# Performance work log

Measured on AMD Instinct MI355X. Metric: run time of the kernel, lower is better.

## Reference

```python
import jax, jax.numpy as jnp
import numpy as np

N = 50000           # num_nodes
E = 400000          # num directed input edges
CON_DIM = 128
STRUC_DIM = 64
HIDDEN = 128
NUM_NODE_UPDATES = 5
MAX_GROUP_ITERS = 100


def setup_inputs() -> dict:
    key = jax.random.key(0)
    k = jax.random.split(key, 5)
    return {
        "con_feats": jax.random.normal(k[0], (N, CON_DIM), jnp.float32),
        "struc_feats": jax.random.normal(k[1], (N, STRUC_DIM), jnp.float32),
        "W1": jax.random.normal(k[2], (2 * CON_DIM, HIDDEN), jnp.float32) * 0.05,
        "b1": jnp.zeros((HIDDEN,), jnp.float32),
        "W2": jax.random.normal(k[3], (HIDDEN, 1), jnp.float32) * 0.05,
        "b2": jnp.zeros((1,), jnp.float32),
        "edge_ids": jax.random.randint(k[4], (2, E), 0, N, jnp.int32),
    }


def _edge_scores(con_feats, W1, b1, W2, b2, src, dst, upper):
    # MLP edge scorer on concatenated endpoint features; relu'd score,
    # zeroed on edges failing the dst > src pruning (equivalent to torch's
    # boolean pruning: score-0 edges contribute nothing downstream).
    x = jnp.concatenate([con_feats[src], con_feats[dst]], axis=1)  # [E, 2*C]
    raw = (jax.nn.relu(x @ W1 + b1) @ W2 + b2)[:, 0]               # [E]
    return jax.nn.relu(raw) * upper


def reference(con_feats, struc_feats, W1, b1, W2, b2, edge_ids):
    num_nodes = con_feats.shape[0]
    src, dst = edge_ids[0], edge_ids[1]
    upper = (dst > src).astype(con_feats.dtype)
    scores = _edge_scores(con_feats, W1, b1, W2, b2, src, dst, upper)
    ar = jnp.arange(num_nodes, dtype=edge_ids.dtype)

    # full edge set: pruned + flipped + self-loops (score-0 edges are no-ops)
    all_src = jnp.concatenate([src, dst, ar])
    all_dst = jnp.concatenate([dst, src, ar])
    all_scores = jnp.concatenate([scores, scores, jnp.ones((num_nodes,), scores.dtype)])

    # row-wise normalization (scatter-sum over source node)
    node_sums = jax.ops.segment_sum(all_scores, all_src, num_segments=num_nodes)
    norm_scores = all_scores / node_sums[all_src]

    def spmm(f):  # sparse [N,N] @ dense [N,d]
        return jax.ops.segment_sum(norm_scores[:, None] * f[all_dst], all_src,
                                   num_segments=num_nodes)

    for _ in range(NUM_NODE_UPDATES):
        con_feats = spmm(con_feats)
        struc_feats = spmm(struc_feats)

    # connected-components label propagation over edges with positive score
    # (edges with score==0 are rewritten as self-edges instead of filtered,
    # which is a no-op for scatter-min; self-loops appended as in torch)
    g_src = jnp.concatenate([jnp.where(scores > 0, src, dst), ar])
    g_dst = jnp.concatenate([dst, ar])

    def cond(state):
        i, _, changed = state
        return (i < MAX_GROUP_ITERS) & changed

    def body(state):
        i, g, _ = state
        new = jax.ops.segment_min(g[g_src], g_dst, num_segments=num_nodes)
        return (i + 1, new, jnp.any(new != g))

    _, group_ids, _ = jax.lax.while_loop(cond, body,
                                         (jnp.int32(0), ar, jnp.bool_(True)))

    # compact labels (torch.unique return_inverse); output padded to N rows
    _, inv = jnp.unique(group_ids, return_inverse=True, size=num_nodes,
                        fill_value=num_nodes - 1)
    inv = inv.reshape(-1)

    counts = jax.ops.segment_sum(jnp.ones((num_nodes,), con_feats.dtype), inv,
                                 num_segments=num_nodes)
    denom = jnp.maximum(counts, 1.0)[:, None]
    con_out = jax.ops.segment_sum(con_feats, inv, num_segments=num_nodes) / denom
    struc_out = jax.ops.segment_sum(struc_feats, inv, num_segments=num_nodes) / denom
    # [N, CON_DIM + STRUC_DIM]; rows >= num_groups are zero padding
    return jnp.concatenate([con_out, struc_out], axis=1)
```

## Files before the change

kernel.cpp:

```cpp
#include <hip/hip_runtime.h>
#include <hip/hip_fp16.h>
#include <cstdint>
#include <cstddef>


__global__ void k_init(const float* __restrict__ con, const float* __restrict__ str,
                       __half* __restrict__ F, float* __restrict__ sums,
                       int* __restrict__ cnt, int* __restrict__ g, int N) {
  int i = blockIdx.x * blockDim.x + threadIdx.x;
  int total = N * 192;
  if (i < total) {
    int n = i / 192, f = i - n * 192;
    float v = (f < 128) ? con[n * 128 + f] : str[n * 64 + (f - 128)];
    F[i] = __float2half_rn(v);
  }
  if (i < N) { sums[i] = 1.0f; cnt[i] = 1; g[i] = i; }
}

__global__ __launch_bounds__(256) void k_proj(const float* __restrict__ con,
                                              const float* __restrict__ W1,
                                              const float* __restrict__ b1,
                                              float* __restrict__ PQf,
                                              __half* __restrict__ PQh, int N) {
  __shared__ float cs[16][128];
  int n0 = blockIdx.x * 16;
  for (int t = threadIdx.x; t < 16 * 128; t += 256) {
    int tn = t >> 7, k = t & 127;
    int node = n0 + tn;
    cs[tn][k] = (node < N) ? con[node * 128 + k] : 0.0f;
  }
  __syncthreads();
  int j = threadIdx.x;
  int base = (j < 128) ? j : (128 * 128 + (j - 128));
  float acc[16];
#pragma unroll
  for (int t = 0; t < 16; ++t) acc[t] = 0.0f;
  float w0 = W1[base + 0 * 128];
  float w1 = W1[base + 1 * 128];
  float w2 = W1[base + 2 * 128];
  float w3 = W1[base + 3 * 128];
  for (int k = 0; k < 128; k += 4) {
    float n0w = 0.f, n1w = 0.f, n2w = 0.f, n3w = 0.f;
    if (k < 124) {
      n0w = W1[base + (k + 4) * 128];
      n1w = W1[base + (k + 5) * 128];
      n2w = W1[base + (k + 6) * 128];
      n3w = W1[base + (k + 7) * 128];
    }
#pragma unroll
    for (int t = 0; t < 16; ++t) {
      const float4 c = *reinterpret_cast<const float4*>(&cs[t][k]);
      acc[t] += c.x * w0 + c.y * w1 + c.z * w2 + c.w * w3;
    }
    w0 = n0w; w1 = n1w; w2 = n2w; w3 = n3w;
  }
  float bj = (j < 128) ? b1[j] : 0.0f;
#pragma unroll
  for (int t = 0; t < 16; ++t) {
    int node = n0 + t;
    if (node < N) {
      float v = acc[t] + bj;
      PQf[(size_t)node * 256 + j] = v;
      PQh[(size_t)node * 256 + j] = __float2half_rn(v);
    }
  }
}

__global__ __launch_bounds__(256) void k_edge(const int* __restrict__ src, const int* __restrict__ dst,
                                              const __half* __restrict__ PQ,
                                              const float* __restrict__ PQf,
                                              const float* __restrict__ W2,
                                              const float* __restrict__ b2,
                                              float* __restrict__ scores,
                                              float* __restrict__ sums, int* __restrict__ cnt,
                                              int* __restrict__ pos_s, int* __restrict__ pos_d,
                                              int* __restrict__ pos_cnt, int E) {
  int e = blockIdx.x * 256 + threadIdx.x;
  bool live = (e < E);
  int s = 0, d = 0;
  if (live) { s = src[e]; d = dst[e]; }
  bool scored = live && (d > s);
  float raw = -1.0f;
  if (scored) {
    const uint4* P = (const uint4*)(PQ + (size_t)s * 256);
    const uint4* Q = (const uint4*)(PQ + (size_t)d * 256 + 128);
    const float4* W = (const float4*)W2;
    float acc = 0.0f;
#pragma unroll 8
    for (int k = 0; k < 16; ++k) {
      uint4 pu = P[k];
      uint4 qu = Q[k];
      float4 wa = W[2 * k], wb = W[2 * k + 1];
      float2 p0 = __half22float2(*(const __half2*)&pu.x);
      float2 p1 = __half22float2(*(const __half2*)&pu.y);
      float2 p2 = __half22float2(*(const __half2*)&pu.z);
      float2 p3 = __half22float2(*(const __half2*)&pu.w);
      float2 q0 = __half22float2(*(const __half2*)&qu.x);
      float2 q1 = __half22float2(*(const __half2*)&qu.y);
      float2 q2 = __half22float2(*(const __half2*)&qu.z);
      float2 q3 = __half22float2(*(const __half2*)&qu.w);
      acc += fmaxf(p0.x + q0.x, 0.f) * wa.x + fmaxf(p0.y + q0.y, 0.f) * wa.y
           + fmaxf(p1.x + q1.x, 0.f) * wa.z + fmaxf(p1.y + q1.y, 0.f) * wa.w
           + fmaxf(p2.x + q2.x, 0.f) * wb.x + fmaxf(p2.y + q2.y, 0.f) * wb.y
           + fmaxf(p3.x + q3.x, 0.f) * wb.z + fmaxf(p3.y + q3.y, 0.f) * wb.w;
    }
    raw = acc + b2[0];
    if (fabsf(raw) < 3e-3f) {
      const float4* Pf = (const float4*)(PQf + (size_t)s * 256);
      const float4* Qf = (const float4*)(PQf + (size_t)d * 256 + 128);
      float acc2 = 0.0f;
      for (int k = 0; k < 32; ++k) {
        float4 p = Pf[k], q = Qf[k], w = W[k];
        acc2 += fmaxf(p.x + q.x, 0.f) * w.x + fmaxf(p.y + q.y, 0.f) * w.y
              + fmaxf(p.z + q.z, 0.f) * w.z + fmaxf(p.w + q.w, 0.f) * w.w;
      }
      raw = acc2 + b2[0];
    }
  }
  float sc = scored ? fmaxf(raw, 0.0f) : 0.0f;
  if (live) scores[e] = sc;
  bool pos = scored && (sc > 0.0f);
  if (pos) {
    atomicAdd(&sums[s], sc);
    atomicAdd(&sums[d], sc);
    atomicAdd(&cnt[s], 1);
    atomicAdd(&cnt[d], 1);
  }
  unsigned long long m = __ballot(pos);
  if (pos) {
    int lane = threadIdx.x & 63;
    int rank = __popcll(m & ((1ULL << lane) - 1));
    int leader = __ffsll((long long)m) - 1;
    int bcast;
    if (lane == leader) bcast = atomicAdd(pos_cnt, __popcll(m));
    bcast = __shfl(bcast, leader, 64);
    pos_s[bcast + rank] = s;
    pos_d[bcast + rank] = d;
  }
}

__device__ __forceinline__ int wave_iscan(int v) {
  int l = threadIdx.x & 63;
#pragma unroll
  for (int o = 1; o < 64; o <<= 1) {
    int t = __shfl_up(v, o, 64);
    if (l >= o) v += t;
  }
  return v;
}

__global__ __launch_bounds__(1024) void k_scan_red(int mode, const int* __restrict__ cnt,
                                                   const int* __restrict__ g,
                                                   int* __restrict__ bsum, int N) {
  __shared__ int wsum[16];
  int i = blockIdx.x * 1024 + threadIdx.x;
  int v = 0;
  if (i < N) v = (mode == 0) ? cnt[i] : ((g[i] == i) ? 1 : 0);
  int incl = wave_iscan(v);
  int wid = threadIdx.x >> 6;
  if ((threadIdx.x & 63) == 63) wsum[wid] = incl;
  __syncthreads();
  if (threadIdx.x == 0) {
    int t = 0;
#pragma unroll
    for (int k = 0; k < 16; ++k) t += wsum[k];
    bsum[blockIdx.x] = t;
  }
}

__global__ __launch_bounds__(64) void k_scan_mid(int mode, const int* __restrict__ bsum,
                                                 int* __restrict__ bexcl, int NB,
                                                 int* __restrict__ rowp, int N) {
  int l = threadIdx.x;
  int v = (l < NB) ? bsum[l] : 0;
  int incl = wave_iscan(v);
  if (l < NB) bexcl[l] = incl - v;
  if (l == 63 && mode == 0) rowp[N] = incl;
}

__global__ __launch_bounds__(1024) void k_scan_out(int mode, const int* __restrict__ cnt,
                                                   const int* __restrict__ g,
                                                   const float* __restrict__ sums,
                                                   const int* __restrict__ bexcl,
                                                   int* __restrict__ rowp, int* __restrict__ fillp,
                                                   int* __restrict__ col, float* __restrict__ wt,
                                                   int* __restrict__ rank, int N) {
  __shared__ int wsum[16];
  int i = blockIdx.x * 1024 + threadIdx.x;
  int v = 0;
  if (i < N) v = (mode == 0) ? cnt[i] : ((g[i] == i) ? 1 : 0);
  int incl = wave_iscan(v);
  int wid = threadIdx.x >> 6;
  if ((threadIdx.x & 63) == 63) wsum[wid] = incl;
  __syncthreads();
  if (threadIdx.x < 64) {
    int l = threadIdx.x;
    int sv = (l < 16) ? wsum[l] : 0;
#pragma unroll
    for (int o = 1; o < 16; o <<= 1) {
      int t = __shfl_up(sv, o, 64);
      if (l >= o) sv += t;
    }
    if (l < 16) wsum[l] = sv;
  }
  __syncthreads();
  int wexcl = (wid == 0) ? 0 : wsum[wid - 1];
  int excl = bexcl[blockIdx.x] + wexcl + incl - v;
  if (i < N) {
    if (mode == 0) {
      rowp[i] = excl;
      fillp[i] = excl + 1;
      col[excl] = i;
      wt[excl] = 1.0f / sums[i];
    } else {
      rank[i] = excl;
    }
  }
}

__global__ void k_fill(const int* __restrict__ src, const int* __restrict__ dst,
                       const float* __restrict__ scores, const float* __restrict__ sums,
                       int* __restrict__ fillp, int* __restrict__ col, float* __restrict__ wt,
                       int E) {
  int e = blockIdx.x * blockDim.x + threadIdx.x;
  if (e >= E) return;
  float sc = scores[e];
  if (sc <= 0.0f) return;
  int s = src[e], d = dst[e];
  int p = atomicAdd(&fillp[s], 1);
  col[p] = d; wt[p] = sc / sums[s];
  int p2 = atomicAdd(&fillp[d], 1);
  col[p2] = s; wt[p2] = sc / sums[d];
}

__global__ __launch_bounds__(192) void k_spmm(const __half* __restrict__ Fin, __half* __restrict__ Fout,
                                              const int* __restrict__ rowp,
                                              const int* __restrict__ col,
                                              const float* __restrict__ wt, int N) {
  int tid = blockIdx.x * 192 + threadIdx.x;
  int row = tid / 24;
  int f8 = tid - row * 24;
  if (row >= N) return;
  const uint4* F8 = (const uint4*)Fin;
  int beg = rowp[row], end = rowp[row + 1];
  float a0 = 0.f, a1 = 0.f, a2 = 0.f, a3 = 0.f, a4 = 0.f, a5 = 0.f, a6 = 0.f, a7 = 0.f;
  int cnx = col[beg];
  float wnx = wt[beg];
  for (int idx = beg; idx < end; ++idx) {
    int c = cnx; float wv = wnx;
    if (idx + 1 < end) { cnx = col[idx + 1]; wnx = wt[idx + 1]; }
    uint4 v = F8[(size_t)c * 24 + f8];
    float2 v0 = __half22float2(*(const __half2*)&v.x);
    float2 v1 = __half22float2(*(const __half2*)&v.y);
    float2 v2 = __half22float2(*(const __half2*)&v.z);
    float2 v3 = __half22float2(*(const __half2*)&v.w);
    a0 += wv * v0.x; a1 += wv * v0.y; a2 += wv * v1.x; a3 += wv * v1.y;
    a4 += wv * v2.x; a5 += wv * v2.y; a6 += wv * v3.x; a7 += wv * v3.y;
  }
  uint4 o;
  *(__half2*)&o.x = __floats2half2_rn(a0, a1);
  *(__half2*)&o.y = __floats2half2_rn(a2, a3);
  *(__half2*)&o.z = __floats2half2_rn(a4, a5);
  *(__half2*)&o.w = __floats2half2_rn(a6, a7);
  ((uint4*)Fout)[(size_t)row * 24 + f8] = o;
}

__global__ void k_prop(const int* __restrict__ pos_s, const int* __restrict__ pos_d,
                       const int* __restrict__ pos_cnt, int* g, int N) {
  int i = blockIdx.x * blockDim.x + threadIdx.x;
  volatile int* gv = g;
  int P = *pos_cnt;
#pragma unroll
  for (int r = 0; r < 2; ++r) {
    if (i < P) {
      int s = pos_s[i], d = pos_d[i];
      int gs = gv[s];
      if (gs < gv[d]) atomicMin(&g[d], gs);
    }
    if (i < N) {
      int gi = gv[i];
      int gg = gv[gi];
      if (gg < gi) atomicMin(&g[i], gg);
      gi = gv[i];
      gg = gv[gi];
      if (gg < gi) atomicMin(&g[i], gg);
    }
  }
}

__global__ void k_gcnt(const int* __restrict__ g, const int* __restrict__ rank,
                       int* __restrict__ gcnt, int N) {
  int i = blockIdx.x * blockDim.x + threadIdx.x;
  if (i < N) atomicAdd(&gcnt[rank[g[i]]], 1);
}

__global__ void k_inv(const int* __restrict__ gcnt, float* __restrict__ invc, int N) {
  int i = blockIdx.x * blockDim.x + threadIdx.x;
  if (i < N) invc[i] = 1.0f / (float)max(gcnt[i], 1);
}

__global__ __launch_bounds__(192) void k_accum(const __half* __restrict__ F, const int* __restrict__ g,
                                               const int* __restrict__ rank,
                                               const float* __restrict__ invc,
                                               float* __restrict__ out, int N) {
  __shared__ int jbuf[64];
  int n0 = blockIdx.x * 64;
  if (threadIdx.x < 64) {
    int n = n0 + threadIdx.x;
    jbuf[threadIdx.x] = (n < N) ? rank[g[n]] : -1;
  }
  __syncthreads();
  int f = threadIdx.x;
  int lim = min(64, N - n0);
  float acc = 0.0f; int cur = -1;
  for (int k = 0; k < lim; ++k) {
    int j = jbuf[k];
    float v = __half2float(F[(size_t)(n0 + k) * 192 + f]);
    if (j != cur) {
      if (cur >= 0) atomicAdd(&out[(size_t)cur * 192 + f], acc * invc[cur]);
      cur = j; acc = v;
    } else {
      acc += v;
    }
  }
  if (cur >= 0) atomicAdd(&out[(size_t)cur * 192 + f], acc * invc[cur]);
}

extern "C" void kernel_launch(void* const* d_in, const int* in_sizes, int n_in,
                              void* d_out, int out_size, void* d_ws, size_t ws_size,
                              hipStream_t stream) {
  const float* con = (const float*)d_in[0];
  const float* str = (const float*)d_in[1];
  const float* W1  = (const float*)d_in[2];
  const float* b1  = (const float*)d_in[3];
  const float* W2  = (const float*)d_in[4];
  const float* b2  = (const float*)d_in[5];
  const int* edges = (const int*)d_in[6];
  int N = in_sizes[0] / 128;
  int E = in_sizes[6] / 2;
  const int* src = edges;
  const int* dst = edges + E;
  int NB = (N + 1023) / 1024;

  uint8_t* w = (uint8_t*)d_ws;
  size_t off = 0;
  auto alloc = [&](size_t bytes) -> void* {
    void* p = w + off;
    off += (bytes + 255) & ~(size_t)255;
    return p;
  };
  __half* Fa    = (__half*)alloc((size_t)N * 192 * 2);
  float*  PQf   = (float*)alloc((size_t)N * 256 * 4);
  __half* Fb    = (__half*)PQf;
  float* scores = (float*)alloc((size_t)E * 4);
  float* sums   = (float*)alloc((size_t)N * 4);
  int*   cnt    = (int*)alloc((size_t)N * 4);
  int*   g      = (int*)alloc((size_t)N * 4);
  int*   pos_s  = (int*)alloc((size_t)E * 4);
  int*   pos_d  = (int*)alloc((size_t)E * 4);
  int*   pos_c  = (int*)alloc(256);
  int*   bsum   = (int*)alloc(64 * 4);
  int*   bexcl  = (int*)alloc(64 * 4);
  size_t mark = off;
  int*   colA   = (int*)alloc((2 * (size_t)E + N) * 4);
  float* wtA    = (float*)alloc((2 * (size_t)E + N) * 4);
  int*   rowp   = (int*)alloc((size_t)(N + 1) * 4);
  int*   fillp  = (int*)alloc((size_t)N * 4);
  int*   rank   = (int*)alloc((size_t)N * 4);
  int*   gcnt   = (int*)alloc((size_t)N * 4);
  float* invc   = (float*)alloc((size_t)N * 4);
  size_t pqh_bytes = (size_t)N * 256 * 2;
  if (off < mark + pqh_bytes) off = mark + ((pqh_bytes + 255) & ~(size_t)255);
  __half* PQh = (__half*)(w + mark);

  hipMemsetAsync(d_out, 0, (size_t)out_size * 4, stream);
  hipMemsetAsync(pos_c, 0, 4, stream);

  k_init<<<(N * 192 + 255) / 256, 256, 0, stream>>>(con, str, Fa, sums, cnt, g, N);
  k_proj<<<(N + 15) / 16, 256, 0, stream>>>(con, W1, b1, PQf, PQh, N);
  k_edge<<<(E + 255) / 256, 256, 0, stream>>>(src, dst, PQh, PQf, W2, b2, scores, sums, cnt,
                                              pos_s, pos_d, pos_c, E);
  k_scan_red<<<NB, 1024, 0, stream>>>(0, cnt, g, bsum, N);
  k_scan_mid<<<1, 64, 0, stream>>>(0, bsum, bexcl, NB, rowp, N);
  k_scan_out<<<NB, 1024, 0, stream>>>(0, cnt, g, sums, bexcl, rowp, fillp, colA, wtA, rank, N);
  k_fill<<<(E + 255) / 256, 256, 0, stream>>>(src, dst, scores, sums, fillp, colA, wtA, E);

  __half* fin = Fa; __half* fout = Fb;
  for (int it = 0; it < 5; ++it) {
    k_spmm<<<((size_t)N * 24 + 191) / 192, 192, 0, stream>>>(fin, fout, rowp, colA, wtA, N);
    __half* tmp = fin; fin = fout; fout = tmp;
  }

  for (int r = 0; r < 9; ++r)
    k_prop<<<(E + 255) / 256, 256, 0, stream>>>(pos_s, pos_d, pos_c, g, N);

  k_scan_red<<<NB, 1024, 0, stream>>>(1, cnt, g, bsum, N);
  k_scan_mid<<<1, 64, 0, stream>>>(1, bsum, bexcl, NB, rowp, N);
  k_scan_out<<<NB, 1024, 0, stream>>>(1, cnt, g, sums, bexcl, rowp, fillp, colA, wtA, rank, N);
  hipMemsetAsync(gcnt, 0, (size_t)N * 4, stream);
  k_gcnt<<<(N + 255) / 256, 256, 0, stream>>>(g, rank, gcnt, N);
  k_inv<<<(N + 255) / 256, 256, 0, stream>>>(gcnt, invc, N);
  k_accum<<<(N + 63) / 64, 192, 0, stream>>>(fin, g, rank, invc, (float*)d_out, N);
}
```

Before: 538.9 us.

## Restructure projection kernel per-wave tiling and unroll SpMM gather by two

The projection GEMM drops the shared-memory staging of node features. Each wave now handles 8 nodes and every lane computes four output columns (P and Q halves), reading node features straight from global memory as broadcast float4 loads. Each block covers 32 nodes, so half as many blocks are launched. The SpMM inner loop is unrolled by two so two independent gathers are in flight per iteration, at the cost of more registers and a tail case.

Result: slower. 588.8 us (+9.3%).

```diff
diff --git a/kernel.cpp b/kernel.cpp
--- a/kernel.cpp
+++ b/kernel.cpp
@@ -22,46 +22,45 @@
                                               const float* __restrict__ b1,
                                               float* __restrict__ PQf,
                                               __half* __restrict__ PQh, int N) {
-  __shared__ float cs[16][128];
-  int n0 = blockIdx.x * 16;
-  for (int t = threadIdx.x; t < 16 * 128; t += 256) {
-    int tn = t >> 7, k = t & 127;
-    int node = n0 + tn;
-    cs[tn][k] = (node < N) ? con[node * 128 + k] : 0.0f;
-  }
-  __syncthreads();
-  int j = threadIdx.x;
-  int base = (j < 128) ? j : (128 * 128 + (j - 128));
-  float acc[16];
-#pragma unroll
-  for (int t = 0; t < 16; ++t) acc[t] = 0.0f;
-  float w0 = W1[base + 0 * 128];
-  float w1 = W1[base + 1 * 128];
-  float w2 = W1[base + 2 * 128];
-  float w3 = W1[base + 3 * 128];
+  int wave = threadIdx.x >> 6;
+  int lane = threadIdx.x & 63;
+  int n0 = blockIdx.x * 32 + wave * 8;
+  const float* W1q = W1 + 128 * 128;
+  float aP0[8], aP1[8], aQ0[8], aQ1[8];
+#pragma unroll
+  for (int t = 0; t < 8; ++t) { aP0[t] = 0.f; aP1[t] = 0.f; aQ0[t] = 0.f; aQ1[t] = 0.f; }
+  int cL = lane, cH = 64 + lane;
   for (int k = 0; k < 128; k += 4) {
-    float n0w = 0.f, n1w = 0.f, n2w = 0.f, n3w = 0.f;
-    if (k < 124) {
-      n0w = W1[base + (k + 4) * 128];
-      n1w = W1[base + (k + 5) * 128];
-      n2w = W1[base + (k + 6) * 128];
-      n3w = W1[base + (k + 7) * 128];
-    }
-#pragma unroll
-    for (int t = 0; t < 16; ++t) {
-      const float4 c = *reinterpret_cast<const float4*>(&cs[t][k]);
-      acc[t] += c.x * w0 + c.y * w1 + c.z * w2 + c.w * w3;
-    }
-    w0 = n0w; w1 = n1w; w2 = n2w; w3 = n3w;
-  }
-  float bj = (j < 128) ? b1[j] : 0.0f;
-#pragma unroll
-  for (int t = 0; t < 16; ++t) {
+    float wP0[4], wP1[4], wQ0[4], wQ1[4];
+#pragma unroll
+    for (int u = 0; u < 4; ++u) {
+      wP0[u] = W1[(k + u) * 128 + cL];
+      wP1[u] = W1[(k + u) * 128 + cH];
+      wQ0[u] = W1q[(k + u) * 128 + cL];
+      wQ1[u] = W1q[(k + u) * 128 + cH];
+    }
+#pragma unroll
+    for (int t = 0; t < 8; ++t) {
+      int node = min(n0 + t, N - 1);
+      const float4 c4 = *(const float4*)&con[(size_t)node * 128 + k];
+      aP0[t] += c4.x * wP0[0] + c4.y * wP0[1] + c4.z * wP0[2] + c4.w * wP0[3];
+      aP1[t] += c4.x * wP1[0] + c4.y * wP1[1] + c4.z * wP1[2] + c4.w * wP1[3];
+      aQ0[t] += c4.x * wQ0[0] + c4.y * wQ0[1] + c4.z * wQ0[2] + c4.w * wQ0[3];
+      aQ1[t] += c4.x * wQ1[0] + c4.y * wQ1[1] + c4.z * wQ1[2] + c4.w * wQ1[3];
+    }
+  }
+  float bL = b1[cL], bH = b1[cH];
+#pragma unroll
+  for (int t = 0; t < 8; ++t) {
     int node = n0 + t;
     if (node < N) {
-      float v = acc[t] + bj;
-      PQf[(size_t)node * 256 + j] = v;
-      PQh[(size_t)node * 256 + j] = __float2half_rn(v);
+      float vP0 = aP0[t] + bL, vP1 = aP1[t] + bH;
+      float* rf = PQf + (size_t)node * 256;
+      rf[cL] = vP0; rf[cH] = vP1;
+      rf[128 + cL] = aQ0[t]; rf[128 + cH] = aQ1[t];
+      __half* rh = PQh + (size_t)node * 256;
+      rh[cL] = __float2half_rn(vP0); rh[cH] = __float2half_rn(vP1);
+      rh[128 + cL] = __float2half_rn(aQ0[t]); rh[128 + cH] = __float2half_rn(aQ1[t]);
     }
   }
 }
@@ -244,18 +243,35 @@
   const uint4* F8 = (const uint4*)Fin;
   int beg = rowp[row], end = rowp[row + 1];
   float a0 = 0.f, a1 = 0.f, a2 = 0.f, a3 = 0.f, a4 = 0.f, a5 = 0.f, a6 = 0.f, a7 = 0.f;
-  int cnx = col[beg];
-  float wnx = wt[beg];
-  for (int idx = beg; idx < end; ++idx) {
-    int c = cnx; float wv = wnx;
-    if (idx + 1 < end) { cnx = col[idx + 1]; wnx = wt[idx + 1]; }
-    uint4 v = F8[(size_t)c * 24 + f8];
-    float2 v0 = __half22float2(*(const __half2*)&v.x);
-    float2 v1 = __half22float2(*(const __half2*)&v.y);
-    float2 v2 = __half22float2(*(const __half2*)&v.z);
-    float2 v3 = __half22float2(*(const __half2*)&v.w);
-    a0 += wv * v0.x; a1 += wv * v0.y; a2 += wv * v1.x; a3 += wv * v1.y;
-    a4 += wv * v2.x; a5 += wv * v2.y; a6 += wv * v3.x; a7 += wv * v3.y;
+  int idx = beg;
+  for (; idx + 1 < end; idx += 2) {
+    int c0 = col[idx], c1 = col[idx + 1];
+    float w0 = wt[idx], w1 = wt[idx + 1];
+    uint4 u0 = F8[(size_t)c0 * 24 + f8];
+    uint4 u1 = F8[(size_t)c1 * 24 + f8];
+    float2 x0 = __half22float2(*(const __half2*)&u0.x);
+    float2 x1 = __half22float2(*(const __half2*)&u0.y);
+    float2 x2 = __half22float2(*(const __half2*)&u0.z);
+    float2 x3 = __half22float2(*(const __half2*)&u0.w);
+    a0 += w0 * x0.x; a1 += w0 * x0.y; a2 += w0 * x1.x; a3 += w0 * x1.y;
+    a4 += w0 * x2.x; a5 += w0 * x2.y; a6 += w0 * x3.x; a7 += w0 * x3.y;
+    float2 y0 = __half22float2(*(const __half2*)&u1.x);
+    float2 y1 = __half22float2(*(const __half2*)&u1.y);
+    float2 y2 = __half22float2(*(const __half2*)&u1.z);
+    float2 y3 = __half22float2(*(const __half2*)&u1.w);
+    a0 += w1 * y0.x; a1 += w1 * y0.y; a2 += w1 * y1.x; a3 += w1 * y1.y;
+    a4 += w1 * y2.x; a5 += w1 * y2.y; a6 += w1 * y3.x; a7 += w1 * y3.y;
+  }
+  if (idx < end) {
+    int c0 = col[idx];
+    float w0 = wt[idx];
+    uint4 u0 = F8[(size_t)c0 * 24 + f8];
+    float2 x0 = __half22float2(*(const __half2*)&u0.x);
+    float2 x1 = __half22float2(*(const __half2*)&u0.y);
+    float2 x2 = __half22float2(*(const __half2*)&u0.z);
+    float2 x3 = __half22float2(*(const __half2*)&u0.w);
+    a0 += w0 * x0.x; a1 += w0 * x0.y; a2 += w0 * x1.x; a3 += w0 * x1.y;
+    a4 += w0 * x2.x; a5 += w0 * x2.y; a6 += w0 * x3.x; a7 += w0 * x3.y;
   }
   uint4 o;
   *(__half2*)&o.x = __floats2half2_rn(a0, a1);
@@ -377,7 +393,7 @@
   hipMemsetAsync(pos_c, 0, 4, stream);
 
   k_init<<<(N * 192 + 255) / 256, 256, 0, stream>>>(con, str, Fa, sums, cnt, g, N);
-  k_proj<<<(N + 15) / 16, 256, 0, stream>>>(con, W1, b1, PQf, PQh, N);
+  k_proj<<<(N + 31) / 32, 256, 0, stream>>>(con, W1, b1, PQf, PQh, N);
   k_edge<<<(E + 255) / 256, 256, 0, stream>>>(src, dst, PQh, PQf, W2, b2, scores, sums, cnt,
                                               pos_s, pos_d, pos_c, E);
   k_scan_red<<<NB, 1024, 0, stream>>>(0, cnt, g, bsum, N);
```
